# Performance work log

Measured on AMD Instinct MI355X. Metric: run time of the kernel, lower is better.

## Reference

```python
import jax, jax.numpy as jnp
import numpy as np

SCALE_POS = 2.0
SCALE_NEG = 40.0
THRESH_POS = 0.5
THRESH_NEG = 0.5
MARGIN = 0.1
EPS = 1e-5


def setup_inputs() -> dict:
    key = jax.random.key(0)
    kf, kl = jax.random.split(key)
    B, D, NUM_CLASSES = 4096, 1024, 64
    feats = jax.random.normal(kf, (B, D), dtype=jnp.float32)
    feats = feats / jnp.linalg.norm(feats, axis=1, keepdims=True)  # L2-normalized embeddings
    labels = jax.random.randint(kl, (B,), 0, NUM_CLASSES, dtype=jnp.int64)
    return {"feats": feats, "labels": labels}


def reference(feats, labels):
    B = feats.shape[0]
    sim = jnp.matmul(feats, feats.T)  # [B, B]
    same = labels[:, None] == labels[None, :]
    pos_mask = same & (sim < 1.0 - EPS)  # drop self / near-duplicate pairs
    neg_mask = ~same

    # hard mining: keep negatives above min positive - margin, positives below max negative + margin
    min_pos = jnp.min(jnp.where(pos_mask, sim, jnp.inf), axis=1)   # [B]
    max_neg = jnp.max(jnp.where(neg_mask, sim, -jnp.inf), axis=1)  # [B]
    neg_sel = neg_mask & (sim + MARGIN > min_pos[:, None])
    pos_sel = pos_mask & (sim - MARGIN < max_neg[:, None])

    pos_sum = jnp.sum(jnp.where(pos_sel, jnp.exp(-SCALE_POS * (sim - THRESH_POS)), 0.0), axis=1)
    neg_sum = jnp.sum(jnp.where(neg_sel, jnp.exp(SCALE_NEG * (sim - THRESH_NEG)), 0.0), axis=1)
    pos_loss = jnp.log1p(pos_sum) / SCALE_POS
    neg_loss = jnp.log1p(neg_sum) / SCALE_NEG

    valid = jnp.any(pos_sel, axis=1) & jnp.any(neg_sel, axis=1)  # rows skipped by original loop
    return jnp.sum(jnp.where(valid, pos_loss + neg_loss, 0.0)) / B
```

## Files before the change

kernel.cpp:

```cpp
#include <hip/hip_runtime.h>

typedef short short8 __attribute__((ext_vector_type(8)));
typedef _Float16 half8 __attribute__((ext_vector_type(8)));
typedef float floatx4 __attribute__((ext_vector_type(4)));
typedef __attribute__((address_space(1))) const void gvoid;
typedef __attribute__((address_space(3))) void svoid;

#define SCALE_POS 2.0f
#define SCALE_NEG 40.0f
#define THRESH 0.5f
#define MARGIN 0.1f
#define EPSV 1e-5f

__device__ __forceinline__ unsigned short f2bf(float f) {
    unsigned u = __float_as_uint(f);
    u += 0x7fffu + ((u >> 16) & 1u);
    return (unsigned short)(u >> 16);
}
__device__ __forceinline__ unsigned f2ord(float f) {
    unsigned u = __float_as_uint(f);
    return (u & 0x80000000u) ? ~u : (u | 0x80000000u);
}
__device__ __forceinline__ float ord2f(unsigned e) {
    unsigned v = (e & 0x80000000u) ? (e & 0x7fffffffu) : ~e;
    return __uint_as_float(v);
}

#define ORD_POS_INF 0xff800000u
#define ORD_NEG_INF 0x007fffffu

__global__ void k_init(const float* __restrict__ feats,
                       unsigned short* __restrict__ fb16,
                       unsigned* __restrict__ minp, unsigned* __restrict__ maxn,
                       float* __restrict__ psum, float* __restrict__ nsum,
                       unsigned* __restrict__ cnts,
                       int total4, int B) {
    int i = blockIdx.x * blockDim.x + threadIdx.x;
    if (i < total4) {
        float4 v = ((const float4*)feats)[i];
        ushort4 o;
        o.x = f2bf(v.x); o.y = f2bf(v.y); o.z = f2bf(v.z); o.w = f2bf(v.w);
        ((ushort4*)fb16)[i] = o;
    }
    if (i < B) {
        minp[i] = ORD_POS_INF;
        maxn[i] = ORD_NEG_INF;
        psum[i] = 0.f;
        nsum[i] = 0.f;
    }
    if (i < 64) cnts[i] = 0;
}

__global__ void __launch_bounds__(256, 4)
k_gemm_ws(const unsigned short* __restrict__ fb16,
          const int* __restrict__ labels,
          unsigned* __restrict__ minp_ord,
          unsigned* __restrict__ maxn_ord,
          _Float16* __restrict__ simh,
          unsigned* __restrict__ tile_cnt,
          int D, int nb, int NT) {
    __shared__ __align__(16) unsigned short As[128 * 32];
    __shared__ __align__(16) unsigned short Bs[128 * 32];
    __shared__ int labR[128], labC[128];
    __shared__ unsigned tshare;

    const int tid = threadIdx.x;
    const int lane = tid & 63;
    const int wave = tid >> 6;
    const int wr = wave >> 1, wc = wave & 1;
    const int q = lane >> 4;
    const int cIn = lane & 15;

    const int c0 = wave * 2, c1 = c0 + 1;
    const int srow = lane >> 2;
    const int scol = (lane & 3) * 8;
    unsigned short* lA0 = As + c0 * 512 + lane * 8;
    unsigned short* lA1 = As + c1 * 512 + lane * 8;
    unsigned short* lB0 = Bs + c0 * 512 + lane * 8;
    unsigned short* lB1 = Bs + c1 * 512 + lane * 8;

    int aOff[4], bOff[4];
#pragma unroll
    for (int i = 0; i < 4; ++i) {
        aOff[i] = (wr * 64 + i * 16 + cIn) * 32 + q * 8;
        bOff[i] = (wc * 64 + i * 16 + cIn) * 32 + q * 8;
    }

    const int KT = D >> 5;

    for (;;) {
        __syncthreads();
        if (tid == 0) tshare = atomicAdd(tile_cnt, 1u);
        __syncthreads();
        const unsigned t = tshare;
        if (t >= (unsigned)NT) break;

        int rb = 0, rem = (int)t;
        while (rem >= nb - rb) { rem -= nb - rb; ++rb; }
        const int cb = rb + rem;
        const int rowBase = rb * 128;
        const int colBase = cb * 128;

        if (tid < 128) labR[tid] = labels[rowBase + tid];
        else           labC[tid - 128] = labels[colBase + tid - 128];

        const unsigned short* gA0 = fb16 + (size_t)(rowBase + c0 * 16 + srow) * D + scol;
        const unsigned short* gA1 = fb16 + (size_t)(rowBase + c1 * 16 + srow) * D + scol;
        const unsigned short* gB0 = fb16 + (size_t)(colBase + c0 * 16 + srow) * D + scol;
        const unsigned short* gB1 = fb16 + (size_t)(colBase + c1 * 16 + srow) * D + scol;

        floatx4 acc[4][4] = {};

        for (int kt = 0; kt < KT; ++kt) {
            const int kOff = kt * 32;
            __syncthreads();
            __builtin_amdgcn_global_load_lds((gvoid*)(gA0 + kOff), (svoid*)lA0, 16, 0, 0);
            __builtin_amdgcn_global_load_lds((gvoid*)(gA1 + kOff), (svoid*)lA1, 16, 0, 0);
            __builtin_amdgcn_global_load_lds((gvoid*)(gB0 + kOff), (svoid*)lB0, 16, 0, 0);
            __builtin_amdgcn_global_load_lds((gvoid*)(gB1 + kOff), (svoid*)lB1, 16, 0, 0);
            __syncthreads();

            short8 a[4], b[4];
#pragma unroll
            for (int i = 0; i < 4; ++i) a[i] = *(const short8*)(As + aOff[i]);
#pragma unroll
            for (int i = 0; i < 4; ++i) b[i] = *(const short8*)(Bs + bOff[i]);
#pragma unroll
            for (int i = 0; i < 4; ++i)
#pragma unroll
                for (int j = 0; j < 4; ++j)
                    acc[i][j] = __builtin_amdgcn_mfma_f32_16x16x32_bf16(a[i], b[j], acc[i][j], 0, 0, 0);
        }

        int rLabv[16];
#pragma unroll
        for (int mi = 0; mi < 4; ++mi)
#pragma unroll
            for (int rr = 0; rr < 4; ++rr)
                rLabv[mi * 4 + rr] = labR[wr * 64 + mi * 16 + q * 4 + rr];
        int cLabv[4];
#pragma unroll
        for (int ni = 0; ni < 4; ++ni)
            cLabv[ni] = labC[wc * 64 + ni * 16 + cIn];

        {
            half8* dst = (half8*)(simh + (size_t)t * 16384 + (size_t)tid * 64);
#pragma unroll
            for (int mi = 0; mi < 4; ++mi) {
                half8 h0, h1;
#pragma unroll
                for (int ni = 0; ni < 2; ++ni)
#pragma unroll
                    for (int rr = 0; rr < 4; ++rr) {
                        h0[ni * 4 + rr] = (_Float16)acc[mi][ni][rr];
                        h1[ni * 4 + rr] = (_Float16)acc[mi][ni + 2][rr];
                    }
                dst[mi * 2] = h0;
                dst[mi * 2 + 1] = h1;
            }
        }

#pragma unroll
        for (int mi = 0; mi < 4; ++mi)
#pragma unroll
            for (int rr = 0; rr < 4; ++rr) {
                const int rLoc = wr * 64 + mi * 16 + q * 4 + rr;
                const int rLab = rLabv[mi * 4 + rr];
                float vmin = 1e30f, vmax = -1e30f;
#pragma unroll
                for (int ni = 0; ni < 4; ++ni) {
                    float s = acc[mi][ni][rr];
                    if (rLab == cLabv[ni]) {
                        if (s < 1.0f - EPSV) vmin = fminf(vmin, s);
                    } else {
                        vmax = fmaxf(vmax, s);
                    }
                }
#pragma unroll
                for (int off = 8; off; off >>= 1) {
                    vmin = fminf(vmin, __shfl_xor(vmin, off, 16));
                    vmax = fmaxf(vmax, __shfl_xor(vmax, off, 16));
                }
                if (cIn == 0) {
                    if (vmin < 1e30f) atomicMin(&minp_ord[rowBase + rLoc], f2ord(vmin));
                    if (vmax > -1e30f) atomicMax(&maxn_ord[rowBase + rLoc], f2ord(vmax));
                }
            }

        if (rb != cb) {
#pragma unroll
            for (int ni = 0; ni < 4; ++ni) {
                const int cLab = cLabv[ni];
                float vmin = 1e30f, vmax = -1e30f;
#pragma unroll
                for (int mi = 0; mi < 4; ++mi)
#pragma unroll
                    for (int rr = 0; rr < 4; ++rr) {
                        float s = acc[mi][ni][rr];
                        if (rLabv[mi * 4 + rr] == cLab) {
                            if (s < 1.0f - EPSV) vmin = fminf(vmin, s);
                        } else {
                            vmax = fmaxf(vmax, s);
                        }
                    }
                vmin = fminf(vmin, __shfl_xor(vmin, 16, 64));
                vmin = fminf(vmin, __shfl_xor(vmin, 32, 64));
                vmax = fmaxf(vmax, __shfl_xor(vmax, 16, 64));
                vmax = fmaxf(vmax, __shfl_xor(vmax, 32, 64));
                if (q == 0) {
                    const int cLoc = wc * 64 + ni * 16 + cIn;
                    if (vmin < 1e30f) atomicMin(&minp_ord[colBase + cLoc], f2ord(vmin));
                    if (vmax > -1e30f) atomicMax(&maxn_ord[colBase + cLoc], f2ord(vmax));
                }
            }
        }
    }
}

__global__ void k_sum2f(const _Float16* __restrict__ simh,
                        const int* __restrict__ labels,
                        const unsigned* __restrict__ minp_ord,
                        const unsigned* __restrict__ maxn_ord,
                        float* __restrict__ psum, float* __restrict__ nsum,
                        unsigned* __restrict__ done_cnt,
                        float* __restrict__ out,
                        int nb, int B) {
    __shared__ int labR[128], labC[128];
    __shared__ float mpR[128], mnR[128], mpC[128], mnC[128];
    __shared__ float red[4];
    __shared__ unsigned lastflag;

    int t = blockIdx.x;
    int rb = 0, rem = t;
    while (rem >= nb - rb) { rem -= nb - rb; ++rb; }
    const int cb = rb + rem;

    const int tid = threadIdx.x;
    const int lane = tid & 63;
    const int wave = tid >> 6;
    const int wr = wave >> 1, wc = wave & 1;
    const int rowBase = rb * 128;
    const int colBase = cb * 128;
    const int q = lane >> 4;
    const int cIn = lane & 15;

    if (tid < 128) {
        labR[tid] = labels[rowBase + tid];
        mpR[tid] = ord2f(minp_ord[rowBase + tid]) - MARGIN;
        mnR[tid] = ord2f(maxn_ord[rowBase + tid]) + MARGIN;
    } else {
        int j = tid - 128;
        labC[j] = labels[colBase + j];
        mpC[j] = ord2f(minp_ord[colBase + j]) - MARGIN;
        mnC[j] = ord2f(maxn_ord[colBase + j]) + MARGIN;
    }
    __syncthreads();

    int cLabv[4];
    float mpCv[4], mnCv[4];
#pragma unroll
    for (int ni = 0; ni < 4; ++ni) {
        const int cLoc = wc * 64 + ni * 16 + cIn;
        cLabv[ni] = labC[cLoc];
        mpCv[ni] = mpC[cLoc];
        mnCv[ni] = mnC[cLoc];
    }

    const half8* src = (const half8*)(simh + (size_t)t * 16384 + (size_t)tid * 64);
    half8 hv[8];
#pragma unroll
    for (int v = 0; v < 8; ++v) hv[v] = src[v];

    float cps[4] = {}, cns[4] = {};
    const bool offd = (rb != cb);

#pragma unroll
    for (int mi = 0; mi < 4; ++mi)
#pragma unroll
        for (int rr = 0; rr < 4; ++rr) {
            const int rLoc = wr * 64 + mi * 16 + q * 4 + rr;
            const int rLab = labR[rLoc];
            const float gateN = mpR[rLoc];
            const float gateP = mnR[rLoc];
            float rp = 0.f, rn = 0.f;
#pragma unroll
            for (int ni = 0; ni < 4; ++ni) {
                const int idx = mi * 16 + ni * 4 + rr;
                const float s = (float)hv[idx >> 3][idx & 7];
                if (rLab == cLabv[ni]) {
                    if (s < 1.0f - EPSV) {
                        float ev = __expf(-SCALE_POS * (s - THRESH));
                        if (s < gateP) rp += ev;
                        if (offd && s < mnCv[ni]) cps[ni] += ev;
                    }
                } else {
                    float ev = __expf(SCALE_NEG * (s - THRESH));
                    if (s > gateN) rn += ev;
                    if (offd && s > mpCv[ni]) cns[ni] += ev;
                }
            }
#pragma unroll
            for (int off = 8; off; off >>= 1) {
                rp += __shfl_xor(rp, off, 16);
                rn += __shfl_xor(rn, off, 16);
            }
            if (cIn == 0) {
                if (rp != 0.f) atomicAdd(&psum[rowBase + rLoc], rp);
                if (rn != 0.f) atomicAdd(&nsum[rowBase + rLoc], rn);
            }
        }
    if (offd) {
#pragma unroll
        for (int ni = 0; ni < 4; ++ni) {
            cps[ni] += __shfl_xor(cps[ni], 16, 64);
            cps[ni] += __shfl_xor(cps[ni], 32, 64);
            cns[ni] += __shfl_xor(cns[ni], 16, 64);
            cns[ni] += __shfl_xor(cns[ni], 32, 64);
            if (q == 0) {
                const int cLoc = wc * 64 + ni * 16 + cIn;
                if (cps[ni] != 0.f) atomicAdd(&psum[colBase + cLoc], cps[ni]);
                if (cns[ni] != 0.f) atomicAdd(&nsum[colBase + cLoc], cns[ni]);
            }
        }
    }

    __syncthreads();
    if (tid == 0) {
        unsigned prev = __hip_atomic_fetch_add(done_cnt, 1u, __ATOMIC_ACQ_REL,
                                               __HIP_MEMORY_SCOPE_AGENT);
        lastflag = (prev == (unsigned)(gridDim.x - 1)) ? 1u : 0u;
    }
    __syncthreads();
    if (lastflag) {
        float a = 0.f;
        for (int i = tid; i < B; i += 256) {
            float pv = atomicAdd(&psum[i], 0.0f);
            float nv = atomicAdd(&nsum[i], 0.0f);
            if (pv > 0.f && nv > 0.f)
                a += log1pf(pv) * (1.0f / SCALE_POS) + log1pf(nv) * (1.0f / SCALE_NEG);
        }
#pragma unroll
        for (int off = 32; off; off >>= 1) a += __shfl_down(a, off, 64);
        if ((tid & 63) == 0) red[tid >> 6] = a;
        __syncthreads();
        if (tid == 0) out[0] = (red[0] + red[1] + red[2] + red[3]) / (float)B;
    }
}

extern "C" void kernel_launch(void* const* d_in, const int* in_sizes, int n_in,
                              void* d_out, int out_size, void* d_ws, size_t ws_size,
                              hipStream_t stream) {
    const float* feats = (const float*)d_in[0];
    const int* labels = (const int*)d_in[1];
    const int B = in_sizes[1];
    const int D = in_sizes[0] / B;
    const int nb = B / 128;
    const int NT = nb * (nb + 1) / 2;
    const int total4 = B * D / 4;

    char* ws = (char*)d_ws;
    unsigned short* fb16 = (unsigned short*)ws;
    size_t off = (size_t)B * D * sizeof(unsigned short);
    unsigned* minp = (unsigned*)(ws + off); off += (size_t)B * 4;
    unsigned* maxn = (unsigned*)(ws + off); off += (size_t)B * 4;
    float* psum = (float*)(ws + off); off += (size_t)B * 4;
    float* nsum = (float*)(ws + off); off += (size_t)B * 4;
    unsigned* cnts = (unsigned*)(ws + off); off += 256;
    _Float16* simh = (_Float16*)(ws + ((off + 255) & ~(size_t)255));
    float* outp = (float*)d_out;

    k_init<<<(total4 + 255) / 256, 256, 0, stream>>>(feats, fb16, minp, maxn,
                                                     psum, nsum, cnts, total4, B);

    k_gemm_ws<<<1024, 256, 0, stream>>>(fb16, labels, minp, maxn, simh,
                                        &cnts[0], D, nb, NT);

    k_sum2f<<<NT, 256, 0, stream>>>(simh, labels, minp, maxn, psum, nsum,
                                    &cnts[1], outp, nb, B);
}
```

Baseline: 154.2 us.

## Split each upper-triangle tile into two half-column blocks with static launch

Each 128x128 upper-triangle tile is now split into two 128x64 halves, each handled by its own 128-thread block. The persistent atomic work-queue GEMM is replaced by a static grid of 2*NT blocks, and the summation kernel is split the same way. The goal is more, smaller blocks for better load balance across CUs and to drop the tile-counter atomics. In exchange, each half-block reloads the full 128-row A panel, which raises A-tile global traffic, and each block does less MFMA work per LDS load.

```diff
diff --git a/kernel.cpp b/kernel.cpp
--- a/kernel.cpp
+++ b/kernel.cpp
@@ -51,208 +51,197 @@
     if (i < 64) cnts[i] = 0;
 }
 
-__global__ void __launch_bounds__(256, 4)
-k_gemm_ws(const unsigned short* __restrict__ fb16,
-          const int* __restrict__ labels,
-          unsigned* __restrict__ minp_ord,
-          unsigned* __restrict__ maxn_ord,
-          _Float16* __restrict__ simh,
-          unsigned* __restrict__ tile_cnt,
-          int D, int nb, int NT) {
+__global__ void __launch_bounds__(128, 2)
+k_gemm_h(const unsigned short* __restrict__ fb16,
+         const int* __restrict__ labels,
+         unsigned* __restrict__ minp_ord,
+         unsigned* __restrict__ maxn_ord,
+         _Float16* __restrict__ simh,
+         int D, int nb) {
     __shared__ __align__(16) unsigned short As[128 * 32];
-    __shared__ __align__(16) unsigned short Bs[128 * 32];
-    __shared__ int labR[128], labC[128];
-    __shared__ unsigned tshare;
+    __shared__ __align__(16) unsigned short Bs[64 * 32];
+    __shared__ int labR[128], labC[64];
+
+    const int bid = blockIdx.x;
+    int t = bid >> 1;
+    const int h = bid & 1;
+    int rb = 0, rem = t;
+    while (rem >= nb - rb) { rem -= nb - rb; ++rb; }
+    const int cb = rb + rem;
+    const int rowBase = rb * 128;
+    const int colBase = cb * 128 + h * 64;
 
     const int tid = threadIdx.x;
     const int lane = tid & 63;
     const int wave = tid >> 6;
-    const int wr = wave >> 1, wc = wave & 1;
     const int q = lane >> 4;
     const int cIn = lane & 15;
 
-    const int c0 = wave * 2, c1 = c0 + 1;
+    labR[tid] = labels[rowBase + tid];
+    if (tid < 64) labC[tid] = labels[colBase + tid];
+
     const int srow = lane >> 2;
     const int scol = (lane & 3) * 8;
-    unsigned short* lA0 = As + c0 * 512 + lane * 8;
-    unsigned short* lA1 = As + c1 * 512 + lane * 8;
-    unsigned short* lB0 = Bs + c0 * 512 + lane * 8;
-    unsigned short* lB1 = Bs + c1 * 512 + lane * 8;
+    const unsigned short* gP[6];
+    unsigned short* lP[6];
+#pragma unroll
+    for (int j = 0; j < 6; ++j) {
+        const int c = wave * 6 + j;
+        const int base = (c < 8) ? (rowBase + c * 16) : (colBase + (c - 8) * 16);
+        gP[j] = fb16 + (size_t)(base + srow) * D + scol;
+        lP[j] = ((c < 8) ? (As + c * 512) : (Bs + (c - 8) * 512)) + lane * 8;
+    }
 
     int aOff[4], bOff[4];
 #pragma unroll
     for (int i = 0; i < 4; ++i) {
-        aOff[i] = (wr * 64 + i * 16 + cIn) * 32 + q * 8;
-        bOff[i] = (wc * 64 + i * 16 + cIn) * 32 + q * 8;
-    }
+        aOff[i] = (wave * 64 + i * 16 + cIn) * 32 + q * 8;
+        bOff[i] = (i * 16 + cIn) * 32 + q * 8;
+    }
+
+    floatx4 acc[4][4] = {};
 
     const int KT = D >> 5;
-
-    for (;;) {
+    for (int kt = 0; kt < KT; ++kt) {
+        const int kOff = kt * 32;
         __syncthreads();
-        if (tid == 0) tshare = atomicAdd(tile_cnt, 1u);
+#pragma unroll
+        for (int j = 0; j < 6; ++j)
+            __builtin_amdgcn_global_load_lds((gvoid*)(gP[j] + kOff), (svoid*)lP[j], 16, 0, 0);
         __syncthreads();
-        const unsigned t = tshare;
-        if (t >= (unsigned)NT) break;
-
-        int rb = 0, rem = (int)t;
-        while (rem >= nb - rb) { rem -= nb - rb; ++rb; }
-        const int cb = rb + rem;
-        const int rowBase = rb * 128;
-        const int colBase = cb * 128;
-
-        if (tid < 128) labR[tid] = labels[rowBase + tid];
-        else           labC[tid - 128] = labels[colBase + tid - 128];
-
-        const unsigned short* gA0 = fb16 + (size_t)(rowBase + c0 * 16 + srow) * D + scol;
-        const unsigned short* gA1 = fb16 + (size_t)(rowBase + c1 * 16 + srow) * D + scol;
-        const unsigned short* gB0 = fb16 + (size_t)(colBase + c0 * 16 + srow) * D + scol;
-        const unsigned short* gB1 = fb16 + (size_t)(colBase + c1 * 16 + srow) * D + scol;
-
-        floatx4 acc[4][4] = {};
-
-        for (int kt = 0; kt < KT; ++kt) {
-            const int kOff = kt * 32;
-            __syncthreads();
-            __builtin_amdgcn_global_load_lds((gvoid*)(gA0 + kOff), (svoid*)lA0, 16, 0, 0);
-            __builtin_amdgcn_global_load_lds((gvoid*)(gA1 + kOff), (svoid*)lA1, 16, 0, 0);
-            __builtin_amdgcn_global_load_lds((gvoid*)(gB0 + kOff), (svoid*)lB0, 16, 0, 0);
-            __builtin_amdgcn_global_load_lds((gvoid*)(gB1 + kOff), (svoid*)lB1, 16, 0, 0);
-            __syncthreads();
-
-            short8 a[4], b[4];
-#pragma unroll
-            for (int i = 0; i < 4; ++i) a[i] = *(const short8*)(As + aOff[i]);
-#pragma unroll
-            for (int i = 0; i < 4; ++i) b[i] = *(const short8*)(Bs + bOff[i]);
-#pragma unroll
-            for (int i = 0; i < 4; ++i)
-#pragma unroll
-                for (int j = 0; j < 4; ++j)
-                    acc[i][j] = __builtin_amdgcn_mfma_f32_16x16x32_bf16(a[i], b[j], acc[i][j], 0, 0, 0);
-        }
-
-        int rLabv[16];
-#pragma unroll
-        for (int mi = 0; mi < 4; ++mi)
-#pragma unroll
-            for (int rr = 0; rr < 4; ++rr)
-                rLabv[mi * 4 + rr] = labR[wr * 64 + mi * 16 + q * 4 + rr];
-        int cLabv[4];
-#pragma unroll
-        for (int ni = 0; ni < 4; ++ni)
-            cLabv[ni] = labC[wc * 64 + ni * 16 + cIn];
-
-        {
-            half8* dst = (half8*)(simh + (size_t)t * 16384 + (size_t)tid * 64);
-#pragma unroll
-            for (int mi = 0; mi < 4; ++mi) {
-                half8 h0, h1;
-#pragma unroll
-                for (int ni = 0; ni < 2; ++ni)
-#pragma unroll
-                    for (int rr = 0; rr < 4; ++rr) {
-                        h0[ni * 4 + rr] = (_Float16)acc[mi][ni][rr];
-                        h1[ni * 4 + rr] = (_Float16)acc[mi][ni + 2][rr];
-                    }
-                dst[mi * 2] = h0;
-                dst[mi * 2 + 1] = h1;
-            }
-        }
-
-#pragma unroll
-        for (int mi = 0; mi < 4; ++mi)
-#pragma unroll
-            for (int rr = 0; rr < 4; ++rr) {
-                const int rLoc = wr * 64 + mi * 16 + q * 4 + rr;
-                const int rLab = rLabv[mi * 4 + rr];
-                float vmin = 1e30f, vmax = -1e30f;
-#pragma unroll
-                for (int ni = 0; ni < 4; ++ni) {
+
+        short8 a[4], b[4];
+#pragma unroll
+        for (int i = 0; i < 4; ++i) a[i] = *(const short8*)(As + aOff[i]);
+#pragma unroll
+        for (int i = 0; i < 4; ++i) b[i] = *(const short8*)(Bs + bOff[i]);
+#pragma unroll
+        for (int i = 0; i < 4; ++i)
+#pragma unroll
+            for (int j = 0; j < 4; ++j)
+                acc[i][j] = __builtin_amdgcn_mfma_f32_16x16x32_bf16(a[i], b[j], acc[i][j], 0, 0, 0);
+    }
+
+    int rLabv[16];
+#pragma unroll
+    for (int mi = 0; mi < 4; ++mi)
+#pragma unroll
+        for (int rr = 0; rr < 4; ++rr)
+            rLabv[mi * 4 + rr] = labR[wave * 64 + mi * 16 + q * 4 + rr];
+    int cLabv[4];
+#pragma unroll
+    for (int ni = 0; ni < 4; ++ni)
+        cLabv[ni] = labC[ni * 16 + cIn];
+
+    {
+        half8* dst = (half8*)(simh + (size_t)bid * 8192 + (size_t)tid * 64);
+#pragma unroll
+        for (int mi = 0; mi < 4; ++mi) {
+            half8 h0, h1;
+#pragma unroll
+            for (int ni = 0; ni < 2; ++ni)
+#pragma unroll
+                for (int rr = 0; rr < 4; ++rr) {
+                    h0[ni * 4 + rr] = (_Float16)acc[mi][ni][rr];
+                    h1[ni * 4 + rr] = (_Float16)acc[mi][ni + 2][rr];
+                }
+            dst[mi * 2] = h0;
+            dst[mi * 2 + 1] = h1;
+        }
+    }
+
+#pragma unroll
+    for (int mi = 0; mi < 4; ++mi)
+#pragma unroll
+        for (int rr = 0; rr < 4; ++rr) {
+            const int rLoc = wave * 64 + mi * 16 + q * 4 + rr;
+            const int rLab = rLabv[mi * 4 + rr];
+            float vmin = 1e30f, vmax = -1e30f;
+#pragma unroll
+            for (int ni = 0; ni < 4; ++ni) {
+                float s = acc[mi][ni][rr];
+                if (rLab == cLabv[ni]) {
+                    if (s < 1.0f - EPSV) vmin = fminf(vmin, s);
+                } else {
+                    vmax = fmaxf(vmax, s);
+                }
+            }
+#pragma unroll
+            for (int off = 8; off; off >>= 1) {
+                vmin = fminf(vmin, __shfl_xor(vmin, off, 16));
+                vmax = fmaxf(vmax, __shfl_xor(vmax, off, 16));
+            }
+            if (cIn == 0) {
+                if (vmin < 1e30f) atomicMin(&minp_ord[rowBase + rLoc], f2ord(vmin));
+                if (vmax > -1e30f) atomicMax(&maxn_ord[rowBase + rLoc], f2ord(vmax));
+            }
+        }
+
+    if (rb != cb) {
+#pragma unroll
+        for (int ni = 0; ni < 4; ++ni) {
+            const int cLab = cLabv[ni];
+            float vmin = 1e30f, vmax = -1e30f;
+#pragma unroll
+            for (int mi = 0; mi < 4; ++mi)
+#pragma unroll
+                for (int rr = 0; rr < 4; ++rr) {
                     float s = acc[mi][ni][rr];
-                    if (rLab == cLabv[ni]) {
+                    if (rLabv[mi * 4 + rr] == cLab) {
                         if (s < 1.0f - EPSV) vmin = fminf(vmin, s);
                     } else {
                         vmax = fmaxf(vmax, s);
                     }
                 }
-#pragma unroll
-                for (int off = 8; off; off >>= 1) {
-                    vmin = fminf(vmin, __shfl_xor(vmin, off, 16));
-                    vmax = fmaxf(vmax, __shfl_xor(vmax, off, 16));
-                }
-                if (cIn == 0) {
-                    if (vmin < 1e30f) atomicMin(&minp_ord[rowBase + rLoc], f2ord(vmin));
-                    if (vmax > -1e30f) atomicMax(&maxn_ord[rowBase + rLoc], f2ord(vmax));
-                }
-            }
-
-        if (rb != cb) {
-#pragma unroll
-            for (int ni = 0; ni < 4; ++ni) {
-                const int cLab = cLabv[ni];
-                float vmin = 1e30f, vmax = -1e30f;
-#pragma unroll
-                for (int mi = 0; mi < 4; ++mi)
-#pragma unroll
-                    for (int rr = 0; rr < 4; ++rr) {
-                        float s = acc[mi][ni][rr];
-                        if (rLabv[mi * 4 + rr] == cLab) {
-                            if (s < 1.0f - EPSV) vmin = fminf(vmin, s);
-                        } else {
-                            vmax = fmaxf(vmax, s);
-                        }
-                    }
-                vmin = fminf(vmin, __shfl_xor(vmin, 16, 64));
-                vmin = fminf(vmin, __shfl_xor(vmin, 32, 64));
-                vmax = fmaxf(vmax, __shfl_xor(vmax, 16, 64));
-                vmax = fmaxf(vmax, __shfl_xor(vmax, 32, 64));
-                if (q == 0) {
-                    const int cLoc = wc * 64 + ni * 16 + cIn;
-                    if (vmin < 1e30f) atomicMin(&minp_ord[colBase + cLoc], f2ord(vmin));
-                    if (vmax > -1e30f) atomicMax(&maxn_ord[colBase + cLoc], f2ord(vmax));
-                }
-            }
-        }
-    }
-}
-
-__global__ void k_sum2f(const _Float16* __restrict__ simh,
-                        const int* __restrict__ labels,
-                        const unsigned* __restrict__ minp_ord,
-                        const unsigned* __restrict__ maxn_ord,
-                        float* __restrict__ psum, float* __restrict__ nsum,
-                        unsigned* __restrict__ done_cnt,
-                        float* __restrict__ out,
-                        int nb, int B) {
-    __shared__ int labR[128], labC[128];
-    __shared__ float mpR[128], mnR[128], mpC[128], mnC[128];
-    __shared__ float red[4];
+            vmin = fminf(vmin, __shfl_xor(vmin, 16, 64));
+            vmin = fminf(vmin, __shfl_xor(vmin, 32, 64));
+            vmax = fmaxf(vmax, __shfl_xor(vmax, 16, 64));
+            vmax = fmaxf(vmax, __shfl_xor(vmax, 32, 64));
+            if (q == 0) {
+                const int cLoc = ni * 16 + cIn;
+                if (vmin < 1e30f) atomicMin(&minp_ord[colBase + cLoc], f2ord(vmin));
+                if (vmax > -1e30f) atomicMax(&maxn_ord[colBase + cLoc], f2ord(vmax));
+            }
+        }
+    }
+}
+
+__global__ void __launch_bounds__(128)
+k_sum2f(const _Float16* __restrict__ simh,
+        const int* __restrict__ labels,
+        const unsigned* __restrict__ minp_ord,
+        const unsigned* __restrict__ maxn_ord,
+        float* __restrict__ psum, float* __restrict__ nsum,
+        unsigned* __restrict__ done_cnt,
+        float* __restrict__ out,
+        int nb, int B) {
+    __shared__ int labR[128], labC[64];
+    __shared__ float mpR[128], mnR[128], mpC[64], mnC[64];
+    __shared__ float red[2];
     __shared__ unsigned lastflag;
 
-    int t = blockIdx.x;
+    const int bid = blockIdx.x;
+    int t = bid >> 1;
+    const int h = bid & 1;
     int rb = 0, rem = t;
     while (rem >= nb - rb) { rem -= nb - rb; ++rb; }
     const int cb = rb + rem;
+    const int rowBase = rb * 128;
+    const int colBase = cb * 128 + h * 64;
 
     const int tid = threadIdx.x;
     const int lane = tid & 63;
     const int wave = tid >> 6;
-    const int wr = wave >> 1, wc = wave & 1;
-    const int rowBase = rb * 128;
-    const int colBase = cb * 128;
     const int q = lane >> 4;
     const int cIn = lane & 15;
 
-    if (tid < 128) {
-        labR[tid] = labels[rowBase + tid];
-        mpR[tid] = ord2f(minp_ord[rowBase + tid]) - MARGIN;
-        mnR[tid] = ord2f(maxn_ord[rowBase + tid]) + MARGIN;
-    } else {
-        int j = tid - 128;
-        labC[j] = labels[colBase + j];
-        mpC[j] = ord2f(minp_ord[colBase + j]) - MARGIN;
-        mnC[j] = ord2f(maxn_ord[colBase + j]) + MARGIN;
+    labR[tid] = labels[rowBase + tid];
+    mpR[tid] = ord2f(minp_ord[rowBase + tid]) - MARGIN;
+    mnR[tid] = ord2f(maxn_ord[rowBase + tid]) + MARGIN;
+    if (tid < 64) {
+        labC[tid] = labels[colBase + tid];
+        mpC[tid] = ord2f(minp_ord[colBase + tid]) - MARGIN;
+        mnC[tid] = ord2f(maxn_ord[colBase + tid]) + MARGIN;
     }
     __syncthreads();
 
@@ -260,13 +249,13 @@
     float mpCv[4], mnCv[4];
 #pragma unroll
     for (int ni = 0; ni < 4; ++ni) {
-        const int cLoc = wc * 64 + ni * 16 + cIn;
+        const int cLoc = ni * 16 + cIn;
         cLabv[ni] = labC[cLoc];
         mpCv[ni] = mpC[cLoc];
         mnCv[ni] = mnC[cLoc];
     }
 
-    const half8* src = (const half8*)(simh + (size_t)t * 16384 + (size_t)tid * 64);
+    const half8* src = (const half8*)(simh + (size_t)bid * 8192 + (size_t)tid * 64);
     half8 hv[8];
 #pragma unroll
     for (int v = 0; v < 8; ++v) hv[v] = src[v];
@@ -278,7 +267,7 @@
     for (int mi = 0; mi < 4; ++mi)
 #pragma unroll
         for (int rr = 0; rr < 4; ++rr) {
-            const int rLoc = wr * 64 + mi * 16 + q * 4 + rr;
+            const int rLoc = wave * 64 + mi * 16 + q * 4 + rr;
             const int rLab = labR[rLoc];
             const float gateN = mpR[rLoc];
             const float gateP = mnR[rLoc];
@@ -317,7 +306,7 @@
             cns[ni] += __shfl_xor(cns[ni], 16, 64);
             cns[ni] += __shfl_xor(cns[ni], 32, 64);
             if (q == 0) {
-                const int cLoc = wc * 64 + ni * 16 + cIn;
+                const int cLoc = ni * 16 + cIn;
                 if (cps[ni] != 0.f) atomicAdd(&psum[colBase + cLoc], cps[ni]);
                 if (cns[ni] != 0.f) atomicAdd(&nsum[colBase + cLoc], cns[ni]);
             }
@@ -333,7 +322,7 @@
     __syncthreads();
     if (lastflag) {
         float a = 0.f;
-        for (int i = tid; i < B; i += 256) {
+        for (int i = tid; i < B; i += 128) {
             float pv = atomicAdd(&psum[i], 0.0f);
             float nv = atomicAdd(&nsum[i], 0.0f);
             if (pv > 0.f && nv > 0.f)
@@ -343,7 +332,7 @@
         for (int off = 32; off; off >>= 1) a += __shfl_down(a, off, 64);
         if ((tid & 63) == 0) red[tid >> 6] = a;
         __syncthreads();
-        if (tid == 0) out[0] = (red[0] + red[1] + red[2] + red[3]) / (float)B;
+        if (tid == 0) out[0] = (red[0] + red[1]) / (float)B;
     }
 }
 
@@ -356,6 +345,7 @@
     const int D = in_sizes[0] / B;
     const int nb = B / 128;
     const int NT = nb * (nb + 1) / 2;
+    const int NH = NT * 2;
     const int total4 = B * D / 4;
 
     char* ws = (char*)d_ws;
@@ -372,9 +362,8 @@
     k_init<<<(total4 + 255) / 256, 256, 0, stream>>>(feats, fb16, minp, maxn,
                                                      psum, nsum, cnts, total4, B);
 
-    k_gemm_ws<<<1024, 256, 0, stream>>>(fb16, labels, minp, maxn, simh,
-                                        &cnts[0], D, nb, NT);
-
-    k_sum2f<<<NT, 256, 0, stream>>>(simh, labels, minp, maxn, psum, nsum,
+    k_gemm_h<<<NH, 128, 0, stream>>>(fb16, labels, minp, maxn, simh, D, nb);
+
+    k_sum2f<<<NH, 128, 0, stream>>>(simh, labels, minp, maxn, psum, nsum,
                                     &cnts[1], outp, nb, B);
 }
```

Result: slower. 170.0 us (+10.2%).
